# Optimization experiments

Hardware: AMD Instinct MI355X
Metric: run time of the kernel (lower is better)

## Reference

```python
import jax, jax.numpy as jnp
import numpy as np

N_NODES = 100000
N_EDGES = 600000
D_IN = 128
D_OUT = 128
N_REL = 16
N_BASES = 8


def setup_inputs() -> dict:
    key = jax.random.key(0)
    ks = jax.random.split(key, 6)
    x = jax.random.normal(ks[0], (N_NODES, D_IN), dtype=jnp.float32)
    edge_index = jax.random.randint(ks[1], (2, N_EDGES), 0, N_NODES, dtype=jnp.int64)
    edge_type = jax.random.randint(ks[2], (N_EDGES,), 0, N_REL, dtype=jnp.int64)
    # xavier-uniform-ish init scales
    b_lim = float(np.sqrt(6.0 / (D_IN + D_OUT)))
    c_lim = float(np.sqrt(6.0 / (N_REL + N_BASES)))
    w_lim = float(np.sqrt(6.0 / (D_IN + D_OUT)))
    bases = jax.random.uniform(ks[3], (N_BASES, D_IN, D_OUT), jnp.float32, -b_lim, b_lim)
    coefficients = jax.random.uniform(ks[4], (N_REL, N_BASES), jnp.float32, -c_lim, c_lim)
    w_self = jax.random.uniform(ks[5], (D_OUT, D_IN), jnp.float32, -w_lim, w_lim)
    return {"x": x, "edge_index": edge_index, "edge_type": edge_type,
            "bases": bases, "coefficients": coefficients, "w_self": w_self}


def reference(x, edge_index, edge_type, bases, coefficients, w_self):
    # self loop: Linear(in, out, bias=False) -> x @ W^T
    out = x @ w_self.T  # [N, D_OUT]
    # relation weights from basis decomposition
    weights = jnp.einsum('rb,bio->rio', coefficients, bases)  # [R, D_IN, D_OUT]
    row, col = edge_index[0], edge_index[1]
    xc = x[col]  # [E, D_IN] gather of source features
    n_rel = weights.shape[0]
    msg = jnp.zeros((xc.shape[0], w_self.shape[0]), dtype=x.dtype)
    # fixed small loop over relations; masked accumulate matches per-relation grouped GEMM
    for r in range(n_rel):
        sel = (edge_type == r)[:, None]
        msg = msg + jnp.where(sel, xc @ weights[r], jnp.zeros((), x.dtype))
    # scatter-add messages to destination rows
    out = out.at[row].add(msg)
    return out
```

## Files before the change

### kernel.cpp

```cpp
#include <hip/hip_runtime.h>

#define NN 100000
#define NE 600000
#define ET (NE + NN)
#define D 128
#define NREL 16
#define SCANB 391

typedef short short8 __attribute__((ext_vector_type(8)));
typedef float f32x4 __attribute__((ext_vector_type(4)));

#define C0 0
#define O0 20
#define CU0 40
#define T0 60

#define WT_OFF 0
#define META_OFF 557056
#define DH_OFF   557568
#define DO_OFF   957568
#define DC_OFF   1357576
#define BS_OFF   1759168
#define SC_OFF   1761168
#define SR_OFF   4561168
#define MP_OFF   7361168
#define XB_OFF   10161168
#define MSGB_OFF 35761168
#define MSGA_OFF 10161168
#define NEED_B   (MSGB_OFF + (size_t)ET * 128 * 2)
#define NEED_A   (MSGA_OFF + (size_t)ET * 128 * 2)

__device__ __forceinline__ unsigned short f2bf(float f) {
  unsigned u = __builtin_bit_cast(unsigned, f);
  u += 0x7fffu + ((u >> 16) & 1u);
  return (unsigned short)(u >> 16);
}

__global__ __launch_bounds__(256) void k_weights(const float* __restrict__ bases,
    const float* __restrict__ coef, const float* __restrict__ w_self,
    unsigned short* __restrict__ wT)
{
  int idx = blockIdx.x * 256 + threadIdx.x;
  int r = idx >> 14;
  int t = idx & 16383;
  float v;
  if (r < 16) {
    int o = t >> 7, i = t & 127;
    float acc = 0.f;
    #pragma unroll
    for (int b = 0; b < 8; ++b)
      acc += coef[r * 8 + b] * bases[b * 16384 + i * 128 + o];
    v = acc;
  } else {
    v = w_self[t];
  }
  wT[idx] = f2bf(v);
}

__global__ __launch_bounds__(256) void k_xcast(const float* __restrict__ x,
    unsigned short* __restrict__ xb)
{
  int i = blockIdx.x * 256 + threadIdx.x;
  if (i >= NN * D / 4) return;
  float4 f = *(const float4*)(x + (size_t)i * 4);
  short8 dummy;
  unsigned short s0 = f2bf(f.x), s1 = f2bf(f.y), s2 = f2bf(f.z), s3 = f2bf(f.w);
  (void)dummy;
  unsigned long long pk = (unsigned long long)s0 | ((unsigned long long)s1 << 16)
                        | ((unsigned long long)s2 << 32) | ((unsigned long long)s3 << 48);
  *(unsigned long long*)(xb + (size_t)i * 4) = pk;
}

__global__ __launch_bounds__(256) void k_hist(const int* __restrict__ ei,
    const int* __restrict__ et, int* __restrict__ meta, int* __restrict__ dstHist)
{
  __shared__ int h[16];
  int tid = threadIdx.x;
  if (tid < 16) h[tid] = 0;
  __syncthreads();
  for (int e = blockIdx.x * 256 + tid; e < NE; e += gridDim.x * 256) {
    atomicAdd(&h[et[e]], 1);
    atomicAdd(&dstHist[ei[e]], 1);
  }
  __syncthreads();
  if (tid < 16) atomicAdd(&meta[C0 + tid], h[tid]);
}

__global__ __launch_bounds__(256) void k_scan1(const int* __restrict__ dstHist,
    int* __restrict__ dstOff, int* __restrict__ blockSums)
{
  __shared__ int sh[256];
  int tid = threadIdx.x;
  int d = blockIdx.x * 256 + tid;
  int v = (d < NN) ? (dstHist[d] + 1) : 0;
  sh[tid] = v;
  __syncthreads();
  #pragma unroll
  for (int ofs = 1; ofs < 256; ofs <<= 1) {
    int t = (tid >= ofs) ? sh[tid - ofs] : 0;
    __syncthreads();
    sh[tid] += t;
    __syncthreads();
  }
  if (d < NN) dstOff[d] = sh[tid] - v;
  if (tid == 255) blockSums[blockIdx.x] = sh[tid];
}

__global__ __launch_bounds__(512) void k_scan2(int* __restrict__ blockSums, int* __restrict__ meta)
{
  __shared__ int sh[SCANB];
  int tid = threadIdx.x;
  if (tid < SCANB) sh[tid] = blockSums[tid];
  __syncthreads();
  if (tid == 0) {
    int run = 0;
    for (int i = 0; i < SCANB; ++i) { int c = sh[i]; sh[i] = run; run += c; }
    meta[C0 + 16] = NN;
    int off = 0, toff = 0;
    for (int r = 0; r <= 16; ++r) {
      meta[O0 + r] = off;
      meta[CU0 + r] = off;
      meta[T0 + r] = toff;
      int c = meta[C0 + r];
      off += c;
      toff += (c + 63) >> 6;
    }
    meta[O0 + 17] = off;
    meta[T0 + 17] = toff;
  }
  __syncthreads();
  if (tid < SCANB) blockSums[tid] = sh[tid];
}

__global__ __launch_bounds__(256) void k_scan3(int* __restrict__ dstOff,
    const int* __restrict__ blockSums, int* __restrict__ dstCursor,
    int* __restrict__ sCol, int* __restrict__ sRow, int* __restrict__ mpos)
{
  int tid = threadIdx.x;
  int d = blockIdx.x * 256 + tid;
  int base = blockSums[blockIdx.x];
  if (d < NN) {
    int o = dstOff[d] + base;
    dstOff[d] = o;
    dstCursor[d] = o + 1;
    sCol[NE + d] = d;
    sRow[NE + d] = d;
    mpos[NE + d] = o;
  }
  if (d == NN) dstOff[NN] = ET;
}

__global__ __launch_bounds__(256) void k_self0(int* __restrict__ sCol, int* __restrict__ sRow)
{
  int n = blockIdx.x * 256 + threadIdx.x;
  if (n < NN) { sCol[NE + n] = n; sRow[NE + n] = n; }
}

__global__ __launch_bounds__(256) void k_scatter(const int* __restrict__ ei, const int* __restrict__ et,
    int* __restrict__ meta, int* __restrict__ sCol, int* __restrict__ sRow,
    int* __restrict__ mpos, int* __restrict__ dstCursor, int doMsg)
{
  __shared__ int h[16], base[16], lh[16];
  int tid = threadIdx.x;
  int start = blockIdx.x * 4096;
  int end = min(NE, start + 4096);
  if (tid < 16) { h[tid] = 0; lh[tid] = 0; }
  __syncthreads();
  for (int e = start + tid; e < end; e += 256)
    atomicAdd(&h[et[e]], 1);
  __syncthreads();
  if (tid < 16) base[tid] = atomicAdd(&meta[CU0 + tid], h[tid]);
  __syncthreads();
  for (int e = start + tid; e < end; e += 256) {
    int r = et[e];
    int row = ei[e];
    int pos = base[r] + atomicAdd(&lh[r], 1);
    sCol[pos] = ei[NE + e];
    sRow[pos] = row;
    if (doMsg) mpos[pos] = atomicAdd(&dstCursor[row], 1);
  }
}

__global__ __launch_bounds__(256) void k_gemm(const float* __restrict__ xf,
    const unsigned short* __restrict__ xb,
    const unsigned short* __restrict__ wT, const int* __restrict__ meta,
    const int* __restrict__ sCol, const int* __restrict__ sRow,
    const int* __restrict__ mpos, unsigned short* __restrict__ msg,
    float* __restrict__ out, int xbf, int msgmode)
{
  __shared__ short As[64 * 17 * 8];
  __shared__ int Rows[64];
  __shared__ int Pos[64];
  int b = blockIdx.x;
  if (b >= meta[T0 + 17]) return;
  int r = 0;
  while (r < 16 && meta[T0 + r + 1] <= b) ++r;
  int tile = b - meta[T0 + r];
  int boff = meta[O0 + r];
  int bcnt = meta[C0 + r];
  int e0 = boff + tile * 64;
  int nrows = min(64, boff + bcnt - e0);

  int tid = threadIdx.x;
  int lane = tid & 63, wave = tid >> 6;
  int q = lane >> 4, l15 = lane & 15;

  const unsigned short* wr = wT + r * 16384;
  short8 bf[2][4];
  #pragma unroll
  for (int ns = 0; ns < 2; ++ns) {
    #pragma unroll
    for (int kk = 0; kk < 4; ++kk) {
      int n = wave * 32 + ns * 16 + l15;
      bf[ns][kk] = *(const short8*)(wr + n * 128 + kk * 32 + q * 8);
    }
  }

  int m = tid >> 2, ug = tid & 3;
  bool valid = m < nrows;
  int c = valid ? sCol[e0 + m] : 0;
  if (xbf) {
    const unsigned short* xr = xb + (size_t)c * 128;
    #pragma unroll
    for (int s = 0; s < 4; ++s) {
      int u = ug * 4 + s;
      short8 pk = (short8)(short)0;
      if (valid) pk = *(const short8*)(xr + u * 8);
      *(short8*)&As[(m * 17 + u) * 8] = pk;
    }
  } else {
    const float* xr = xf + (size_t)c * 128;
    #pragma unroll
    for (int s = 0; s < 4; ++s) {
      int u = ug * 4 + s;
      float4 f0 = make_float4(0.f, 0.f, 0.f, 0.f), f1 = f0;
      if (valid) {
        f0 = *(const float4*)(xr + u * 8);
        f1 = *(const float4*)(xr + u * 8 + 4);
      }
      short8 pk;
      pk[0] = (short)f2bf(f0.x); pk[1] = (short)f2bf(f0.y);
      pk[2] = (short)f2bf(f0.z); pk[3] = (short)f2bf(f0.w);
      pk[4] = (short)f2bf(f1.x); pk[5] = (short)f2bf(f1.y);
      pk[6] = (short)f2bf(f1.z); pk[7] = (short)f2bf(f1.w);
      *(short8*)&As[(m * 17 + u) * 8] = pk;
    }
  }
  if (tid < 64) {
    Rows[tid] = (tid < nrows) ? sRow[e0 + tid] : 0;
    Pos[tid] = (msgmode && tid < nrows) ? mpos[e0 + tid] : 0;
  }
  __syncthreads();

  f32x4 acc[4][2];
  #pragma unroll
  for (int ms = 0; ms < 4; ++ms)
    #pragma unroll
    for (int ns = 0; ns < 2; ++ns)
      acc[ms][ns] = (f32x4){0.f, 0.f, 0.f, 0.f};

  #pragma unroll
  for (int kk = 0; kk < 4; ++kk) {
    short8 af[4];
    #pragma unroll
    for (int ms = 0; ms < 4; ++ms)
      af[ms] = *(const short8*)&As[((ms * 16 + l15) * 17 + kk * 4 + q) * 8];
    #pragma unroll
    for (int ms = 0; ms < 4; ++ms)
      #pragma unroll
      for (int ns = 0; ns < 2; ++ns)
        acc[ms][ns] = __builtin_amdgcn_mfma_f32_16x16x32_bf16(af[ms], bf[ns][kk], acc[ms][ns], 0, 0, 0);
  }

  if (msgmode) {
    #pragma unroll
    for (int ms = 0; ms < 4; ++ms) {
      #pragma unroll
      for (int reg = 0; reg < 4; ++reg) {
        int mrow = ms * 16 + q * 4 + reg;
        if (mrow < nrows) {
          unsigned short* mp = msg + (size_t)Pos[mrow] * 128 + wave * 32 + l15;
          __builtin_nontemporal_store(f2bf(acc[ms][0][reg]), mp);
          __builtin_nontemporal_store(f2bf(acc[ms][1][reg]), mp + 16);
        }
      }
    }
  } else {
    #pragma unroll
    for (int ms = 0; ms < 4; ++ms) {
      #pragma unroll
      for (int reg = 0; reg < 4; ++reg) {
        int mrow = ms * 16 + q * 4 + reg;
        if (mrow < nrows) {
          float* op = out + (size_t)Rows[mrow] * 128 + wave * 32 + l15;
          unsafeAtomicAdd(op, acc[ms][0][reg]);
          unsafeAtomicAdd(op + 16, acc[ms][1][reg]);
        }
      }
    }
  }
}

__global__ __launch_bounds__(256) void k_reduce(const unsigned short* __restrict__ msg,
    const int* __restrict__ dstOff, float* __restrict__ out)
{
  int d = blockIdx.x * 4 + (threadIdx.x >> 6);
  if (d >= NN) return;
  int lane = threadIdx.x & 63;
  int s = dstOff[d], e = dstOff[d + 1];
  const unsigned int* base = (const unsigned int*)msg;
  float a0 = 0.f, a1 = 0.f, b0 = 0.f, b1 = 0.f;
  int j = s;
  for (; j + 1 < e; j += 2) {
    unsigned int v0 = __builtin_nontemporal_load(base + (size_t)j * 64 + lane);
    unsigned int v1 = __builtin_nontemporal_load(base + (size_t)(j + 1) * 64 + lane);
    a0 += __builtin_bit_cast(float, v0 << 16);
    a1 += __builtin_bit_cast(float, v0 & 0xffff0000u);
    b0 += __builtin_bit_cast(float, v1 << 16);
    b1 += __builtin_bit_cast(float, v1 & 0xffff0000u);
  }
  if (j < e) {
    unsigned int v0 = __builtin_nontemporal_load(base + (size_t)j * 64 + lane);
    a0 += __builtin_bit_cast(float, v0 << 16);
    a1 += __builtin_bit_cast(float, v0 & 0xffff0000u);
  }
  float2 w; w.x = a0 + b0; w.y = a1 + b1;
  *(float2*)(out + (size_t)d * 128 + lane * 2) = w;
}

extern "C" void kernel_launch(void* const* d_in, const int* in_sizes, int n_in,
                              void* d_out, int out_size, void* d_ws, size_t ws_size,
                              hipStream_t stream)
{
  const float* x      = (const float*)d_in[0];
  const int*   ei     = (const int*)d_in[1];
  const int*   et     = (const int*)d_in[2];
  const float* bases  = (const float*)d_in[3];
  const float* coef   = (const float*)d_in[4];
  const float* w_self = (const float*)d_in[5];
  float* out = (float*)d_out;
  char* ws = (char*)d_ws;
  unsigned short* wT = (unsigned short*)(ws + WT_OFF);
  int* meta      = (int*)(ws + META_OFF);
  int* dstHist   = (int*)(ws + DH_OFF);
  int* dstOff    = (int*)(ws + DO_OFF);
  int* dstCursor = (int*)(ws + DC_OFF);
  int* blockSums = (int*)(ws + BS_OFF);
  int* sCol      = (int*)(ws + SC_OFF);
  int* sRow      = (int*)(ws + SR_OFF);
  int* mpos      = (int*)(ws + MP_OFF);
  unsigned short* xb = (unsigned short*)(ws + XB_OFF);

  const int modeB = (ws_size >= NEED_B) ? 1 : 0;
  const int modeA = (modeB || ws_size >= NEED_A) ? 1 : 0;
  unsigned short* msg = (unsigned short*)(ws + (modeB ? MSGB_OFF : MSGA_OFF));

  hipMemsetAsync(ws + META_OFF, 0, 512 + 400000, stream);
  k_weights<<<(17 * 16384) / 256, 256, 0, stream>>>(bases, coef, w_self, wT);
  if (modeB)
    k_xcast<<<(NN * D / 4 + 255) / 256, 256, 0, stream>>>(x, xb);
  k_hist<<<256, 256, 0, stream>>>(ei, et, meta, dstHist);
  if (modeA) {
    k_scan1<<<SCANB, 256, 0, stream>>>(dstHist, dstOff, blockSums);
    k_scan2<<<1, 512, 0, stream>>>(blockSums, meta);
    k_scan3<<<SCANB, 256, 0, stream>>>(dstOff, blockSums, dstCursor, sCol, sRow, mpos);
  } else {
    k_scan2<<<1, 512, 0, stream>>>(blockSums, meta);
    k_self0<<<SCANB, 256, 0, stream>>>(sCol, sRow);
    hipMemsetAsync(d_out, 0, (size_t)NN * D * 4, stream);
  }
  k_scatter<<<(NE + 4095) / 4096, 256, 0, stream>>>(ei, et, meta, sCol, sRow, mpos, dstCursor, modeA);
  k_gemm<<<10954, 256, 0, stream>>>(x, xb, wT, meta, sCol, sRow, mpos, msg, out, modeB, modeA);
  if (modeA)
    k_reduce<<<(NN + 3) / 4, 256, 0, stream>>>(msg, dstOff, out);
}
```

Before: 391.5 us.

## Process several tiles per GEMM block, pack col/pos, stage message stores via LDS

The GEMM kernel now handles four 64-edge tiles per block and reloads the relation weight fragments only when the relation changes. The separate column and message-position index arrays are merged into one int2 array, and row indices are written only in the atomic fallback path. Message output is staged through shared memory so each row goes out as a coalesced 16-byte store instead of scattered 2-byte nontemporal stores. The reduce kernel switches from nontemporal to ordinary loads. In exchange there are fewer blocks in flight, which lowers parallelism and latency hiding, and extra barriers per tile.

```diff
diff --git a/kernel.cpp b/kernel.cpp
--- a/kernel.cpp
+++ b/kernel.cpp
@@ -6,6 +6,9 @@
 #define D 128
 #define NREL 16
 #define SCANB 391
+#define TPB 4
+#define MAXTILES 10954
+#define GEMMG ((MAXTILES + TPB - 1) / TPB)
 
 typedef short short8 __attribute__((ext_vector_type(8)));
 typedef float f32x4 __attribute__((ext_vector_type(4)));
@@ -15,18 +18,17 @@
 #define CU0 40
 #define T0 60
 
-#define WT_OFF 0
+#define WT_OFF   0
 #define META_OFF 557056
 #define DH_OFF   557568
 #define DO_OFF   957568
 #define DC_OFF   1357576
-#define BS_OFF   1759168
-#define SC_OFF   1761168
-#define SR_OFF   4561168
-#define MP_OFF   7361168
-#define XB_OFF   10161168
-#define MSGB_OFF 35761168
-#define MSGA_OFF 10161168
+#define BS_OFF   1757576
+#define SCP_OFF  1759576
+#define SR_OFF   7360088
+#define XB_OFF   10160096
+#define MSGB_OFF 35760096
+#define MSGA_OFF 10160096
 #define NEED_B   (MSGB_OFF + (size_t)ET * 128 * 2)
 #define NEED_A   (MSGA_OFF + (size_t)ET * 128 * 2)
 
@@ -63,9 +65,7 @@
   int i = blockIdx.x * 256 + threadIdx.x;
   if (i >= NN * D / 4) return;
   float4 f = *(const float4*)(x + (size_t)i * 4);
-  short8 dummy;
   unsigned short s0 = f2bf(f.x), s1 = f2bf(f.y), s2 = f2bf(f.z), s3 = f2bf(f.w);
-  (void)dummy;
   unsigned long long pk = (unsigned long long)s0 | ((unsigned long long)s1 << 16)
                         | ((unsigned long long)s2 << 32) | ((unsigned long long)s3 << 48);
   *(unsigned long long*)(xb + (size_t)i * 4) = pk;
@@ -134,7 +134,7 @@
 
 __global__ __launch_bounds__(256) void k_scan3(int* __restrict__ dstOff,
     const int* __restrict__ blockSums, int* __restrict__ dstCursor,
-    int* __restrict__ sCol, int* __restrict__ sRow, int* __restrict__ mpos)
+    int2* __restrict__ sCP)
 {
   int tid = threadIdx.x;
   int d = blockIdx.x * 256 + tid;
@@ -143,22 +143,20 @@
     int o = dstOff[d] + base;
     dstOff[d] = o;
     dstCursor[d] = o + 1;
-    sCol[NE + d] = d;
-    sRow[NE + d] = d;
-    mpos[NE + d] = o;
+    sCP[NE + d] = make_int2(d, o);
   }
   if (d == NN) dstOff[NN] = ET;
 }
 
-__global__ __launch_bounds__(256) void k_self0(int* __restrict__ sCol, int* __restrict__ sRow)
+__global__ __launch_bounds__(256) void k_self0(int2* __restrict__ sCP, int* __restrict__ sRow)
 {
   int n = blockIdx.x * 256 + threadIdx.x;
-  if (n < NN) { sCol[NE + n] = n; sRow[NE + n] = n; }
+  if (n < NN) { sCP[NE + n] = make_int2(n, 0); sRow[NE + n] = n; }
 }
 
 __global__ __launch_bounds__(256) void k_scatter(const int* __restrict__ ei, const int* __restrict__ et,
-    int* __restrict__ meta, int* __restrict__ sCol, int* __restrict__ sRow,
-    int* __restrict__ mpos, int* __restrict__ dstCursor, int doMsg)
+    int* __restrict__ meta, int2* __restrict__ sCP, int* __restrict__ sRow,
+    int* __restrict__ dstCursor, int doMsg)
 {
   __shared__ int h[16], base[16], lh[16];
   int tid = threadIdx.x;
@@ -175,128 +173,140 @@
     int r = et[e];
     int row = ei[e];
     int pos = base[r] + atomicAdd(&lh[r], 1);
-    sCol[pos] = ei[NE + e];
-    sRow[pos] = row;
-    if (doMsg) mpos[pos] = atomicAdd(&dstCursor[row], 1);
+    int slot = doMsg ? atomicAdd(&dstCursor[row], 1) : 0;
+    sCP[pos] = make_int2(ei[NE + e], slot);
+    if (!doMsg) sRow[pos] = row;
   }
 }
 
 __global__ __launch_bounds__(256) void k_gemm(const float* __restrict__ xf,
     const unsigned short* __restrict__ xb,
     const unsigned short* __restrict__ wT, const int* __restrict__ meta,
-    const int* __restrict__ sCol, const int* __restrict__ sRow,
-    const int* __restrict__ mpos, unsigned short* __restrict__ msg,
-    float* __restrict__ out, int xbf, int msgmode)
+    const int2* __restrict__ sCP, const int* __restrict__ sRow,
+    unsigned short* __restrict__ msg, float* __restrict__ out,
+    int xbf, int msgmode)
 {
   __shared__ short As[64 * 17 * 8];
+  __shared__ int Pos[64];
   __shared__ int Rows[64];
-  __shared__ int Pos[64];
-  int b = blockIdx.x;
-  if (b >= meta[T0 + 17]) return;
-  int r = 0;
-  while (r < 16 && meta[T0 + r + 1] <= b) ++r;
-  int tile = b - meta[T0 + r];
-  int boff = meta[O0 + r];
-  int bcnt = meta[C0 + r];
-  int e0 = boff + tile * 64;
-  int nrows = min(64, boff + bcnt - e0);
-
+
+  int ntiles = meta[T0 + 17];
   int tid = threadIdx.x;
   int lane = tid & 63, wave = tid >> 6;
   int q = lane >> 4, l15 = lane & 15;
-
-  const unsigned short* wr = wT + r * 16384;
-  short8 bf[2][4];
-  #pragma unroll
-  for (int ns = 0; ns < 2; ++ns) {
+  int m = tid >> 2, ug = tid & 3;
+
+  int rprev = -1;
+  short8 bfr[2][4];
+
+  for (int ti = 0; ti < TPB; ++ti) {
+    int b = blockIdx.x * TPB + ti;
+    if (b >= ntiles) break;
+    int r = 0;
+    while (r < 16 && meta[T0 + r + 1] <= b) ++r;
+    int tile = b - meta[T0 + r];
+    int boff = meta[O0 + r];
+    int e0 = boff + tile * 64;
+    int nrows = min(64, boff + meta[C0 + r] - e0);
+
+    bool valid = m < nrows;
+    int e = valid ? (e0 + m) : e0;
+    int2 cp = sCP[e];
+    if (ug == 0) {
+      Pos[m] = valid ? cp.y : 0;
+      if (!msgmode) Rows[m] = valid ? sRow[e] : 0;
+    }
+    int c = cp.x;
+    if (xbf) {
+      const unsigned short* xr = xb + (size_t)c * 128;
+      #pragma unroll
+      for (int s = 0; s < 4; ++s) {
+        int u = ug * 4 + s;
+        short8 pk = (short8)(short)0;
+        if (valid) pk = *(const short8*)(xr + u * 8);
+        *(short8*)&As[(m * 17 + u) * 8] = pk;
+      }
+    } else {
+      const float* xr = xf + (size_t)c * 128;
+      #pragma unroll
+      for (int s = 0; s < 4; ++s) {
+        int u = ug * 4 + s;
+        float4 f0 = make_float4(0.f, 0.f, 0.f, 0.f), f1 = f0;
+        if (valid) {
+          f0 = *(const float4*)(xr + u * 8);
+          f1 = *(const float4*)(xr + u * 8 + 4);
+        }
+        short8 pk;
+        pk[0] = (short)f2bf(f0.x); pk[1] = (short)f2bf(f0.y);
+        pk[2] = (short)f2bf(f0.z); pk[3] = (short)f2bf(f0.w);
+        pk[4] = (short)f2bf(f1.x); pk[5] = (short)f2bf(f1.y);
+        pk[6] = (short)f2bf(f1.z); pk[7] = (short)f2bf(f1.w);
+        *(short8*)&As[(m * 17 + u) * 8] = pk;
+      }
+    }
+    __syncthreads();
+
+    if (r != rprev) {
+      const unsigned short* wr = wT + r * 16384;
+      #pragma unroll
+      for (int ns = 0; ns < 2; ++ns)
+        #pragma unroll
+        for (int kk = 0; kk < 4; ++kk)
+          bfr[ns][kk] = *(const short8*)(wr + (wave * 32 + ns * 16 + l15) * 128 + kk * 32 + q * 8);
+      rprev = r;
+    }
+
+    f32x4 acc[4][2];
+    #pragma unroll
+    for (int ms = 0; ms < 4; ++ms)
+      #pragma unroll
+      for (int ns = 0; ns < 2; ++ns)
+        acc[ms][ns] = (f32x4){0.f, 0.f, 0.f, 0.f};
     #pragma unroll
     for (int kk = 0; kk < 4; ++kk) {
-      int n = wave * 32 + ns * 16 + l15;
-      bf[ns][kk] = *(const short8*)(wr + n * 128 + kk * 32 + q * 8);
-    }
-  }
-
-  int m = tid >> 2, ug = tid & 3;
-  bool valid = m < nrows;
-  int c = valid ? sCol[e0 + m] : 0;
-  if (xbf) {
-    const unsigned short* xr = xb + (size_t)c * 128;
-    #pragma unroll
-    for (int s = 0; s < 4; ++s) {
-      int u = ug * 4 + s;
-      short8 pk = (short8)(short)0;
-      if (valid) pk = *(const short8*)(xr + u * 8);
-      *(short8*)&As[(m * 17 + u) * 8] = pk;
-    }
-  } else {
-    const float* xr = xf + (size_t)c * 128;
-    #pragma unroll
-    for (int s = 0; s < 4; ++s) {
-      int u = ug * 4 + s;
-      float4 f0 = make_float4(0.f, 0.f, 0.f, 0.f), f1 = f0;
-      if (valid) {
-        f0 = *(const float4*)(xr + u * 8);
-        f1 = *(const float4*)(xr + u * 8 + 4);
+      short8 af[4];
+      #pragma unroll
+      for (int ms = 0; ms < 4; ++ms)
+        af[ms] = *(const short8*)&As[((ms * 16 + l15) * 17 + kk * 4 + q) * 8];
+      #pragma unroll
+      for (int ms = 0; ms < 4; ++ms)
+        #pragma unroll
+        for (int ns = 0; ns < 2; ++ns)
+          acc[ms][ns] = __builtin_amdgcn_mfma_f32_16x16x32_bf16(af[ms], bfr[ns][kk], acc[ms][ns], 0, 0, 0);
+    }
+
+    if (msgmode) {
+      __syncthreads();
+      #pragma unroll
+      for (int ms = 0; ms < 4; ++ms)
+        #pragma unroll
+        for (int ns = 0; ns < 2; ++ns)
+          #pragma unroll
+          for (int reg = 0; reg < 4; ++reg)
+            As[(ms * 16 + q * 4 + reg) * 136 + wave * 32 + ns * 16 + l15] =
+                (short)f2bf(acc[ms][ns][reg]);
+      __syncthreads();
+      #pragma unroll
+      for (int i = 0; i < 4; ++i) {
+        int row = wave * 16 + i * 4 + (lane >> 4);
+        short8 v = *(const short8*)&As[row * 136 + (lane & 15) * 8];
+        if (row < nrows)
+          *(short8*)(msg + (size_t)Pos[row] * 128 + (lane & 15) * 8) = v;
       }
-      short8 pk;
-      pk[0] = (short)f2bf(f0.x); pk[1] = (short)f2bf(f0.y);
-      pk[2] = (short)f2bf(f0.z); pk[3] = (short)f2bf(f0.w);
-      pk[4] = (short)f2bf(f1.x); pk[5] = (short)f2bf(f1.y);
-      pk[6] = (short)f2bf(f1.z); pk[7] = (short)f2bf(f1.w);
-      *(short8*)&As[(m * 17 + u) * 8] = pk;
-    }
-  }
-  if (tid < 64) {
-    Rows[tid] = (tid < nrows) ? sRow[e0 + tid] : 0;
-    Pos[tid] = (msgmode && tid < nrows) ? mpos[e0 + tid] : 0;
-  }
-  __syncthreads();
-
-  f32x4 acc[4][2];
-  #pragma unroll
-  for (int ms = 0; ms < 4; ++ms)
-    #pragma unroll
-    for (int ns = 0; ns < 2; ++ns)
-      acc[ms][ns] = (f32x4){0.f, 0.f, 0.f, 0.f};
-
-  #pragma unroll
-  for (int kk = 0; kk < 4; ++kk) {
-    short8 af[4];
-    #pragma unroll
-    for (int ms = 0; ms < 4; ++ms)
-      af[ms] = *(const short8*)&As[((ms * 16 + l15) * 17 + kk * 4 + q) * 8];
-    #pragma unroll
-    for (int ms = 0; ms < 4; ++ms)
-      #pragma unroll
-      for (int ns = 0; ns < 2; ++ns)
-        acc[ms][ns] = __builtin_amdgcn_mfma_f32_16x16x32_bf16(af[ms], bf[ns][kk], acc[ms][ns], 0, 0, 0);
-  }
-
-  if (msgmode) {
-    #pragma unroll
-    for (int ms = 0; ms < 4; ++ms) {
-      #pragma unroll
-      for (int reg = 0; reg < 4; ++reg) {
-        int mrow = ms * 16 + q * 4 + reg;
-        if (mrow < nrows) {
-          unsigned short* mp = msg + (size_t)Pos[mrow] * 128 + wave * 32 + l15;
-          __builtin_nontemporal_store(f2bf(acc[ms][0][reg]), mp);
-          __builtin_nontemporal_store(f2bf(acc[ms][1][reg]), mp + 16);
+      __syncthreads();
+    } else {
+      #pragma unroll
+      for (int ms = 0; ms < 4; ++ms)
+        #pragma unroll
+        for (int reg = 0; reg < 4; ++reg) {
+          int mrow = ms * 16 + q * 4 + reg;
+          if (mrow < nrows) {
+            float* op = out + (size_t)Rows[mrow] * 128 + wave * 32 + l15;
+            unsafeAtomicAdd(op, acc[ms][0][reg]);
+            unsafeAtomicAdd(op + 16, acc[ms][1][reg]);
+          }
         }
-      }
-    }
-  } else {
-    #pragma unroll
-    for (int ms = 0; ms < 4; ++ms) {
-      #pragma unroll
-      for (int reg = 0; reg < 4; ++reg) {
-        int mrow = ms * 16 + q * 4 + reg;
-        if (mrow < nrows) {
-          float* op = out + (size_t)Rows[mrow] * 128 + wave * 32 + l15;
-          unsafeAtomicAdd(op, acc[ms][0][reg]);
-          unsafeAtomicAdd(op + 16, acc[ms][1][reg]);
-        }
-      }
+      __syncthreads();
     }
   }
 }
@@ -312,15 +322,15 @@
   float a0 = 0.f, a1 = 0.f, b0 = 0.f, b1 = 0.f;
   int j = s;
   for (; j + 1 < e; j += 2) {
-    unsigned int v0 = __builtin_nontemporal_load(base + (size_t)j * 64 + lane);
-    unsigned int v1 = __builtin_nontemporal_load(base + (size_t)(j + 1) * 64 + lane);
+    unsigned int v0 = base[(size_t)j * 64 + lane];
+    unsigned int v1 = base[(size_t)(j + 1) * 64 + lane];
     a0 += __builtin_bit_cast(float, v0 << 16);
     a1 += __builtin_bit_cast(float, v0 & 0xffff0000u);
     b0 += __builtin_bit_cast(float, v1 << 16);
     b1 += __builtin_bit_cast(float, v1 & 0xffff0000u);
   }
   if (j < e) {
-    unsigned int v0 = __builtin_nontemporal_load(base + (size_t)j * 64 + lane);
+    unsigned int v0 = base[(size_t)j * 64 + lane];
     a0 += __builtin_bit_cast(float, v0 << 16);
     a1 += __builtin_bit_cast(float, v0 & 0xffff0000u);
   }
@@ -346,9 +356,8 @@
   int* dstOff    = (int*)(ws + DO_OFF);
   int* dstCursor = (int*)(ws + DC_OFF);
   int* blockSums = (int*)(ws + BS_OFF);
-  int* sCol      = (int*)(ws + SC_OFF);
+  int2* sCP      = (int2*)(ws + SCP_OFF);
   int* sRow      = (int*)(ws + SR_OFF);
-  int* mpos      = (int*)(ws + MP_OFF);
   unsigned short* xb = (unsigned short*)(ws + XB_OFF);
 
   const int modeB = (ws_size >= NEED_B) ? 1 : 0;
@@ -363,14 +372,14 @@
   if (modeA) {
     k_scan1<<<SCANB, 256, 0, stream>>>(dstHist, dstOff, blockSums);
     k_scan2<<<1, 512, 0, stream>>>(blockSums, meta);
-    k_scan3<<<SCANB, 256, 0, stream>>>(dstOff, blockSums, dstCursor, sCol, sRow, mpos);
+    k_scan3<<<SCANB, 256, 0, stream>>>(dstOff, blockSums, dstCursor, sCP);
   } else {
     k_scan2<<<1, 512, 0, stream>>>(blockSums, meta);
-    k_self0<<<SCANB, 256, 0, stream>>>(sCol, sRow);
+    k_self0<<<SCANB, 256, 0, stream>>>(sCP, sRow);
     hipMemsetAsync(d_out, 0, (size_t)NN * D * 4, stream);
   }
-  k_scatter<<<(NE + 4095) / 4096, 256, 0, stream>>>(ei, et, meta, sCol, sRow, mpos, dstCursor, modeA);
-  k_gemm<<<10954, 256, 0, stream>>>(x, xb, wT, meta, sCol, sRow, mpos, msg, out, modeB, modeA);
+  k_scatter<<<(NE + 4095) / 4096, 256, 0, stream>>>(ei, et, meta, sCP, sRow, dstCursor, modeA);
+  k_gemm<<<GEMMG, 256, 0, stream>>>(x, xb, wT, meta, sCP, sRow, msg, out, modeB, modeA);
   if (modeA)
     k_reduce<<<(NN + 3) / 4, 256, 0, stream>>>(msg, dstOff, out);
 }
```

After: 334.0 us. 14.7% less time.
